# Kernel optimization log

Hardware: AMD Instinct MI355X
Metric: run time of the kernel (lower is better)

## Reference

```python
import jax, jax.numpy as jnp
import numpy as np

N_NODES = 100000
N_EDGES = 1200000
DIM = 64


def _gcn_layer(h, src, dst, norm, W, b):
    # GCNConv: linear -> gather -> normalize -> scatter-add -> bias
    n = h.shape[0]
    h = h @ W                              # [N, D]
    msg = h[src] * norm[:, None]           # [E+N, D] gathered edge messages
    out = jax.ops.segment_sum(msg, dst, num_segments=n)
    return out + b


def setup_inputs() -> dict:
    key = jax.random.key(0)
    ks = jax.random.split(key, 8)
    s = 1.0 / np.sqrt(DIM)
    return {
        "x": jax.random.normal(ks[0], (N_NODES, DIM), jnp.float32),
        "edge_index": jax.random.randint(ks[1], (2, N_EDGES), 0, N_NODES, dtype=jnp.int32),
        "W1": jax.random.normal(ks[2], (DIM, DIM), jnp.float32) * s,
        "b1": jnp.zeros((DIM,), jnp.float32),
        "W2": jax.random.normal(ks[3], (DIM, DIM), jnp.float32) * s,
        "b2": jnp.zeros((DIM,), jnp.float32),
        "W3": jax.random.normal(ks[4], (DIM, DIM), jnp.float32) * s,
        "b3": jnp.zeros((DIM,), jnp.float32),
    }


def reference(x, edge_index, W1, b1, W2, b2, W3, b3):
    n = x.shape[0]
    loops = jnp.arange(n, dtype=edge_index.dtype)
    src = jnp.concatenate([edge_index[0], loops])   # add self-loops (PyG GCNConv default)
    dst = jnp.concatenate([edge_index[1], loops])
    # symmetric degree normalization: norm_e = d^-1/2[src] * d^-1/2[dst]
    deg = jax.ops.segment_sum(jnp.ones(src.shape, x.dtype), dst, num_segments=n)
    dinv = jnp.where(deg > 0, jax.lax.rsqrt(deg), 0.0)
    norm = dinv[src] * dinv[dst]
    h = jax.nn.relu(_gcn_layer(x, src, dst, norm, W1, b1))   # dropout inactive at eval
    h = jax.nn.relu(_gcn_layer(h, src, dst, norm, W2, b2))
    return _gcn_layer(h, src, dst, norm, W3, b3)
```

## Files before the change

### kernel.cpp

```cpp
#include <hip/hip_runtime.h>
#include <math.h>

#define N_NODES 100000
#define N_EDGES 1200000
#define DIM 64
#define ELL_STRIDE 48
#define BNODES 128
#define NBUCKET ((N_NODES + BNODES - 1) / BNODES)
#define BIN_SHIFT 10
#define NBIN ((N_NODES + 1023) >> 10)
#define BIN_CAP 16384
#define CAP 40
#define BIN_BLOCKS 512
#define EPB ((N_EDGES + BIN_BLOCKS - 1) / BIN_BLOCKS)
#define GEMM_BLOCKS ((N_NODES + 63) / 64)
#define GW_BLOCKS (N_NODES / 16)

#define PACK(s, dloc) (((unsigned)(dloc) << 17) | (unsigned)(s))
#define UNPACK_S(p)   ((int)((p) & 0x1FFFF))
#define UNPACK_D(p)   ((int)((p) >> 17))

__device__ __forceinline__ unsigned short f2bf(float f) {
    union { float f; unsigned int u; } v; v.f = f;
    unsigned int r = v.u + 0x7FFF + ((v.u >> 16) & 1);
    return (unsigned short)(r >> 16);
}
__device__ __forceinline__ float bf2f(unsigned short us) {
    return __uint_as_float((unsigned int)us << 16);
}


__global__ void k_init(int* __restrict__ tail) {
    if (threadIdx.x < NBIN) tail[threadIdx.x * 16] = 0;
}


__device__ __forceinline__ void gemm_block(int bid, const float* __restrict__ x,
                                           const float* __restrict__ W,
                                           unsigned short* __restrict__ h,
                                           float4* __restrict__ Xlds) {
    const int tid = threadIdx.x;
    const int lane = tid & 63;

    float wreg[64];
#pragma unroll
    for (int k = 0; k < 64; ++k) wreg[k] = W[k * DIM + lane];

    const int base = bid * 64;
#pragma unroll
    for (int it = 0; it < 4; ++it) {
        int f = tid + it * 256;
        int row = base + (f >> 4);
        if (row >= N_NODES) row = N_NODES - 1;
        Xlds[f] = ((const float4*)x)[row * 16 + (f & 15)];
    }
    __syncthreads();

    const int m0 = (tid >> 6) * 16;
    for (int m = 0; m < 16; ++m) {
        const float4* xr = &Xlds[(m0 + m) * 16];
        float a0 = 0.f, a1 = 0.f, a2 = 0.f, a3 = 0.f;
#pragma unroll
        for (int k4 = 0; k4 < 16; ++k4) {
            float4 xv = xr[k4];
            a0 = fmaf(xv.x, wreg[k4 * 4 + 0], a0);
            a1 = fmaf(xv.y, wreg[k4 * 4 + 1], a1);
            a2 = fmaf(xv.z, wreg[k4 * 4 + 2], a2);
            a3 = fmaf(xv.w, wreg[k4 * 4 + 3], a3);
        }
        int row = base + m0 + m;
        if (row < N_NODES)
            h[(size_t)row * DIM + lane] = f2bf((a0 + a1) + (a2 + a3));
    }
}


__global__ void __launch_bounds__(256) k_pre(const int* __restrict__ ei,
                                             const float* __restrict__ x,
                                             const float* __restrict__ W1,
                                             int* __restrict__ tail,
                                             unsigned* __restrict__ part,
                                             unsigned short* __restrict__ h) {
    __shared__ __align__(16) char smraw[16384];
    __shared__ int lcnt[NBIN];
    __shared__ int gbase[NBIN];
    __shared__ int gcnt[NBIN];

    if (blockIdx.x < GEMM_BLOCKS) {
        gemm_block(blockIdx.x, x, W1, h, (float4*)smraw);
        return;
    }
    unsigned* stg = (unsigned*)smraw;
    const int tid = threadIdx.x;
    for (int i = tid; i < NBIN; i += 256) lcnt[i] = 0;
    __syncthreads();

    const int e0 = (blockIdx.x - GEMM_BLOCKS) * EPB;
    const int eend = (e0 + EPB < N_EDGES) ? e0 + EPB : N_EDGES;
    for (int e = e0 + tid; e < eend; e += 256) {
        int s = ei[e], d = ei[N_EDGES + e];
        int bin = d >> BIN_SHIFT;
        unsigned pk = PACK(s, d & 1023);
        int pos = atomicAdd(&lcnt[bin], 1);
        if (pos < CAP) {
            stg[bin * CAP + pos] = pk;
        } else {
            int gp = atomicAdd(&tail[bin * 16], 1);
            part[(size_t)bin * BIN_CAP + gp] = pk;
        }
    }
    __syncthreads();
    if (tid < NBIN) {
        int c = lcnt[tid]; if (c > CAP) c = CAP;
        gcnt[tid] = c;
        gbase[tid] = c ? atomicAdd(&tail[tid * 16], c) : 0;
    }
    __syncthreads();
    const int wv = tid >> 6, ln = tid & 63;
    for (int b = wv; b < NBIN; b += 4) {
        int c = gcnt[b];
        size_t gbb = (size_t)b * BIN_CAP + gbase[b];
        for (int i = ln; i < c; i += 64)
            part[gbb + i] = stg[b * CAP + i];
    }
}


__global__ void __launch_bounds__(256) k_bucket(const unsigned* __restrict__ part,
                                                const int* __restrict__ tail,
                                                int* __restrict__ ell,
                                                int* __restrict__ deg,
                                                unsigned short* __restrict__ hA,
                                                unsigned short* __restrict__ hB) {
    __shared__ int lcur[BNODES];
    __shared__ int lell[BNODES * ELL_STRIDE];
    const int bucket = blockIdx.x;
    const int tid = threadIdx.x;

    for (int i = tid; i < BNODES; i += 256) lcur[i] = 0;
    __syncthreads();

    const int bin = bucket >> 3;
    const int sub = bucket & 7;
    const int n = tail[bin * 16];
    const unsigned* pb = part + (size_t)bin * BIN_CAP;
    const int node0 = bucket * BNODES;
    for (int i = tid; i < n; i += 256) {
        unsigned p = pb[i];
        unsigned ld = (unsigned)(UNPACK_D(p) - (sub << 7));
        if (ld < BNODES) {
            int pos = atomicAdd(&lcur[ld], 1);
            if (pos < ELL_STRIDE) lell[ld * ELL_STRIDE + pos] = UNPACK_S(p);
        }
    }
    __syncthreads();

    for (int idx = tid; idx < BNODES * ELL_STRIDE; idx += 256) {
        int ln = idx / ELL_STRIDE, sl = idx - ln * ELL_STRIDE;
        int dg = lcur[ln];
        int pe = (dg + 7) & ~7;
        if (pe < 16) pe = 16;
        if (sl >= dg && sl < pe) lell[idx] = N_NODES;
    }
    __syncthreads();

    int4* dst4 = (int4*)(ell + (size_t)bucket * BNODES * ELL_STRIDE);
    const int4* src4 = (const int4*)lell;
    for (int i = tid; i < BNODES * ELL_STRIDE / 4; i += 256) dst4[i] = src4[i];
    for (int i = tid; i < BNODES; i += 256) deg[node0 + i] = lcur[i];

    for (int i = tid; i < BNODES * 8; i += 256) {
        int ln = i >> 3;
        int node = node0 + ln;
        if (node < N_NODES) {
            float dd = rsqrtf((float)(lcur[ln] + 1));
            uint4* p = (uint4*)(hA + (size_t)node * DIM) + (i & 7);
            uint4 v = *p;
            float lo, hi;
            lo = __uint_as_float(v.x << 16) * dd; hi = __uint_as_float(v.x & 0xFFFF0000u) * dd;
            v.x = (unsigned)f2bf(lo) | ((unsigned)f2bf(hi) << 16);
            lo = __uint_as_float(v.y << 16) * dd; hi = __uint_as_float(v.y & 0xFFFF0000u) * dd;
            v.y = (unsigned)f2bf(lo) | ((unsigned)f2bf(hi) << 16);
            lo = __uint_as_float(v.z << 16) * dd; hi = __uint_as_float(v.z & 0xFFFF0000u) * dd;
            v.z = (unsigned)f2bf(lo) | ((unsigned)f2bf(hi) << 16);
            lo = __uint_as_float(v.w << 16) * dd; hi = __uint_as_float(v.w & 0xFFFF0000u) * dd;
            v.w = (unsigned)f2bf(lo) | ((unsigned)f2bf(hi) << 16);
            *p = v;
        }
    }
    if (bucket == 0) {
        if (tid < 8)  ((uint4*)(hA + (size_t)N_NODES * DIM))[tid] = make_uint4(0, 0, 0, 0);
        else if (tid < 16) ((uint4*)(hB + (size_t)N_NODES * DIM))[tid - 8] = make_uint4(0, 0, 0, 0);
    }
}


__global__ void __launch_bounds__(256, 4)
k_gatherW(const unsigned short* __restrict__ h,
          const int* __restrict__ deg,
          const int* __restrict__ ell,
          const float* __restrict__ bvec,
          const float* __restrict__ W,
          unsigned short* __restrict__ hout) {
    __shared__ float sh[16 * 64];
    const int tid = threadIdx.x;
    const int lane = tid & 63;
    const int wv = tid >> 6;
    const int base = blockIdx.x * 16;
    const float bl = bvec[lane];

#pragma unroll 2
    for (int m = 0; m < 4; ++m) {
        int node = base + wv * 4 + m;
        int dg = __builtin_amdgcn_readfirstlane(deg[node]);
        const int* row = ell + (size_t)node * ELL_STRIDE;

        int4 e0 = ((const int4*)row)[0];
        int4 e1 = ((const int4*)row)[1];
        int4 e2 = ((const int4*)row)[2];
        int4 e3 = ((const int4*)row)[3];
        float own = bf2f(h[(size_t)node * DIM + lane]);

        float v0  = bf2f(h[(size_t)e0.x * DIM + lane]);
        float v1  = bf2f(h[(size_t)e0.y * DIM + lane]);
        float v2  = bf2f(h[(size_t)e0.z * DIM + lane]);
        float v3  = bf2f(h[(size_t)e0.w * DIM + lane]);
        float v4  = bf2f(h[(size_t)e1.x * DIM + lane]);
        float v5  = bf2f(h[(size_t)e1.y * DIM + lane]);
        float v6  = bf2f(h[(size_t)e1.z * DIM + lane]);
        float v7  = bf2f(h[(size_t)e1.w * DIM + lane]);
        float v8  = bf2f(h[(size_t)e2.x * DIM + lane]);
        float v9  = bf2f(h[(size_t)e2.y * DIM + lane]);
        float v10 = bf2f(h[(size_t)e2.z * DIM + lane]);
        float v11 = bf2f(h[(size_t)e2.w * DIM + lane]);
        float v12 = bf2f(h[(size_t)e3.x * DIM + lane]);
        float v13 = bf2f(h[(size_t)e3.y * DIM + lane]);
        float v14 = bf2f(h[(size_t)e3.z * DIM + lane]);
        float v15 = bf2f(h[(size_t)e3.w * DIM + lane]);

        float acc = ((own + v0) + (v1 + v2)) + ((v3 + v4) + (v5 + v6))
                  + ((v7 + v8) + (v9 + v10)) + ((v11 + v12) + ((v13 + v14) + v15));

        if (dg > 16) {
            int pe = (dg + 7) & ~7;
            for (int k = 16; k < pe; k += 8) {
                int4 a = *(const int4*)(row + k);
                int4 c = *(const int4*)(row + k + 4);
                float w0 = bf2f(h[(size_t)a.x * DIM + lane]);
                float w1 = bf2f(h[(size_t)a.y * DIM + lane]);
                float w2 = bf2f(h[(size_t)a.z * DIM + lane]);
                float w3 = bf2f(h[(size_t)a.w * DIM + lane]);
                float w4 = bf2f(h[(size_t)c.x * DIM + lane]);
                float w5 = bf2f(h[(size_t)c.y * DIM + lane]);
                float w6 = bf2f(h[(size_t)c.z * DIM + lane]);
                float w7 = bf2f(h[(size_t)c.w * DIM + lane]);
                acc += ((w0 + w1) + (w2 + w3)) + ((w4 + w5) + (w6 + w7));
            }
        }

        float dd = rsqrtf((float)(dg + 1));
        float o = fmaxf(fmaf(acc, dd, bl), 0.f);
        sh[(wv * 4 + m) * 64 + lane] = o;
    }

    float wreg[64];
#pragma unroll
    for (int k = 0; k < 64; ++k) wreg[k] = W[k * DIM + lane];

#pragma unroll
    for (int m = 0; m < 4; ++m) {
        const float4* xr = (const float4*)&sh[(wv * 4 + m) * 64];
        float a0 = 0.f, a1 = 0.f, a2 = 0.f, a3 = 0.f;
#pragma unroll
        for (int k4 = 0; k4 < 16; ++k4) {
            float4 xv = xr[k4];
            a0 = fmaf(xv.x, wreg[k4 * 4 + 0], a0);
            a1 = fmaf(xv.y, wreg[k4 * 4 + 1], a1);
            a2 = fmaf(xv.z, wreg[k4 * 4 + 2], a2);
            a3 = fmaf(xv.w, wreg[k4 * 4 + 3], a3);
        }
        int rown = base + wv * 4 + m;
        float res = (a0 + a1) + (a2 + a3);
        res *= rsqrtf((float)(deg[rown] + 1));
        hout[(size_t)rown * DIM + lane] = f2bf(res);
    }
}


__global__ void k_gatherF(const unsigned short* __restrict__ h,
                          const int* __restrict__ deg,
                          const int* __restrict__ ell, const float* __restrict__ b,
                          float* __restrict__ out) {
    int node = blockIdx.x * 4 + (threadIdx.x >> 6);
    const int lane = threadIdx.x & 63;
    int dg = __builtin_amdgcn_readfirstlane(deg[node]);
    const int* row = ell + (size_t)node * ELL_STRIDE;

    int4 e0 = ((const int4*)row)[0];
    int4 e1 = ((const int4*)row)[1];
    int4 e2 = ((const int4*)row)[2];
    int4 e3 = ((const int4*)row)[3];
    float own = bf2f(h[(size_t)node * DIM + lane]);

    float v0  = bf2f(h[(size_t)e0.x * DIM + lane]);
    float v1  = bf2f(h[(size_t)e0.y * DIM + lane]);
    float v2  = bf2f(h[(size_t)e0.z * DIM + lane]);
    float v3  = bf2f(h[(size_t)e0.w * DIM + lane]);
    float v4  = bf2f(h[(size_t)e1.x * DIM + lane]);
    float v5  = bf2f(h[(size_t)e1.y * DIM + lane]);
    float v6  = bf2f(h[(size_t)e1.z * DIM + lane]);
    float v7  = bf2f(h[(size_t)e1.w * DIM + lane]);
    float v8  = bf2f(h[(size_t)e2.x * DIM + lane]);
    float v9  = bf2f(h[(size_t)e2.y * DIM + lane]);
    float v10 = bf2f(h[(size_t)e2.z * DIM + lane]);
    float v11 = bf2f(h[(size_t)e2.w * DIM + lane]);
    float v12 = bf2f(h[(size_t)e3.x * DIM + lane]);
    float v13 = bf2f(h[(size_t)e3.y * DIM + lane]);
    float v14 = bf2f(h[(size_t)e3.z * DIM + lane]);
    float v15 = bf2f(h[(size_t)e3.w * DIM + lane]);

    float acc = ((own + v0) + (v1 + v2)) + ((v3 + v4) + (v5 + v6))
              + ((v7 + v8) + (v9 + v10)) + ((v11 + v12) + ((v13 + v14) + v15));

    if (dg > 16) {
        int pe = (dg + 7) & ~7;
        for (int k = 16; k < pe; k += 8) {
            int4 a = *(const int4*)(row + k);
            int4 c = *(const int4*)(row + k + 4);
            float w0 = bf2f(h[(size_t)a.x * DIM + lane]);
            float w1 = bf2f(h[(size_t)a.y * DIM + lane]);
            float w2 = bf2f(h[(size_t)a.z * DIM + lane]);
            float w3 = bf2f(h[(size_t)a.w * DIM + lane]);
            float w4 = bf2f(h[(size_t)c.x * DIM + lane]);
            float w5 = bf2f(h[(size_t)c.y * DIM + lane]);
            float w6 = bf2f(h[(size_t)c.z * DIM + lane]);
            float w7 = bf2f(h[(size_t)c.w * DIM + lane]);
            acc += ((w0 + w1) + (w2 + w3)) + ((w4 + w5) + (w6 + w7));
        }
    }

    float dd = rsqrtf((float)(dg + 1));
    out[(size_t)node * DIM + lane] = fmaf(acc, dd, b[lane]);
}


extern "C" void kernel_launch(void* const* d_in, const int* in_sizes, int n_in,
                              void* d_out, int out_size, void* d_ws, size_t ws_size,
                              hipStream_t stream) {
    const float* x   = (const float*)d_in[0];
    const int*   ei  = (const int*)d_in[1];
    const float* W1  = (const float*)d_in[2];
    const float* b1  = (const float*)d_in[3];
    const float* W2  = (const float*)d_in[4];
    const float* b2  = (const float*)d_in[5];
    const float* W3  = (const float*)d_in[6];
    const float* b3  = (const float*)d_in[7];
    float* out = (float*)d_out;

    char* ws = (char*)d_ws;
    int*            deg   = (int*)ws;
    int*            tailp = (int*)(ws + 0x70000);
    int*            ell   = (int*)(ws + 0xD00000);
    unsigned short* hbufA = (unsigned short*)(ws + 0x2000000);
    unsigned short* hbufB = (unsigned short*)(ws + 0x2D00000);
    unsigned*       part  = (unsigned*)(ws + 0x2D00000);

    k_init<<<1, 128, 0, stream>>>(tailp);

    k_pre<<<GEMM_BLOCKS + BIN_BLOCKS, 256, 0, stream>>>(ei, x, W1, tailp, part, hbufA);
    k_bucket<<<NBUCKET, 256, 0, stream>>>(part, tailp, ell, deg, hbufA, hbufB);

    k_gatherW<<<GW_BLOCKS, 256, 0, stream>>>(hbufA, deg, ell, b1, W2, hbufB);
    k_gatherW<<<GW_BLOCKS, 256, 0, stream>>>(hbufB, deg, ell, b2, W3, hbufA);
    k_gatherF<<<N_NODES / 4, 256, 0, stream>>>(hbufA, deg, ell, b3, out);
}
```

Before: 267.5 us.

## Use bf16x3 MFMA for fused GEMM and pre-scaled ELL byte offsets

The per-node dense 64x64 transform in the fused gather kernel is replaced by split-bf16 (hi/lo) MFMA 16x16x32 instructions, with the aggregated rows staged in XOR-swizzled LDS. Precision is kept close to fp32 by adding three cross terms. ELL entries now hold pre-shifted byte offsets (index<<7), so the gather loads skip the 64-bit multiply and address arithmetic. This cuts VALU work and register pressure from the 64-element weight register array. The cost is an extra barrier and the bf16 split conversion overhead.

Result: faster. 246.0 us (-8.0%).

```diff
diff --git a/kernel.cpp b/kernel.cpp
--- a/kernel.cpp
+++ b/kernel.cpp
@@ -20,6 +20,9 @@
 #define UNPACK_S(p)   ((int)((p) & 0x1FFFF))
 #define UNPACK_D(p)   ((int)((p) >> 17))
 
+typedef __attribute__((ext_vector_type(8))) short bf16x8;
+typedef __attribute__((ext_vector_type(4))) float f32x4;
+
 __device__ __forceinline__ unsigned short f2bf(float f) {
     union { float f; unsigned int u; } v; v.f = f;
     unsigned int r = v.u + 0x7FFF + ((v.u >> 16) & 1);
@@ -28,6 +31,8 @@
 __device__ __forceinline__ float bf2f(unsigned short us) {
     return __uint_as_float((unsigned int)us << 16);
 }
+
+#define LDH(boff) bf2f(*(const unsigned short*)((const char*)h + ((unsigned)(boff) + bo)))
 
 
 __global__ void k_init(int* __restrict__ tail) {
@@ -150,7 +155,7 @@
         unsigned ld = (unsigned)(UNPACK_D(p) - (sub << 7));
         if (ld < BNODES) {
             int pos = atomicAdd(&lcur[ld], 1);
-            if (pos < ELL_STRIDE) lell[ld * ELL_STRIDE + pos] = UNPACK_S(p);
+            if (pos < ELL_STRIDE) lell[ld * ELL_STRIDE + pos] = UNPACK_S(p) << 7;
         }
     }
     __syncthreads();
@@ -160,7 +165,7 @@
         int dg = lcur[ln];
         int pe = (dg + 7) & ~7;
         if (pe < 16) pe = 16;
-        if (sl >= dg && sl < pe) lell[idx] = N_NODES;
+        if (sl >= dg && sl < pe) lell[idx] = N_NODES << 7;
     }
     __syncthreads();
 
@@ -202,12 +207,13 @@
           const float* __restrict__ bvec,
           const float* __restrict__ W,
           unsigned short* __restrict__ hout) {
-    __shared__ float sh[16 * 64];
+    __shared__ unsigned short shb[2048];
     const int tid = threadIdx.x;
     const int lane = tid & 63;
     const int wv = tid >> 6;
     const int base = blockIdx.x * 16;
     const float bl = bvec[lane];
+    const unsigned bo = 2u * (unsigned)lane;
 
 #pragma unroll 2
     for (int m = 0; m < 4; ++m) {
@@ -219,24 +225,24 @@
         int4 e1 = ((const int4*)row)[1];
         int4 e2 = ((const int4*)row)[2];
         int4 e3 = ((const int4*)row)[3];
-        float own = bf2f(h[(size_t)node * DIM + lane]);
-
-        float v0  = bf2f(h[(size_t)e0.x * DIM + lane]);
-        float v1  = bf2f(h[(size_t)e0.y * DIM + lane]);
-        float v2  = bf2f(h[(size_t)e0.z * DIM + lane]);
-        float v3  = bf2f(h[(size_t)e0.w * DIM + lane]);
-        float v4  = bf2f(h[(size_t)e1.x * DIM + lane]);
-        float v5  = bf2f(h[(size_t)e1.y * DIM + lane]);
-        float v6  = bf2f(h[(size_t)e1.z * DIM + lane]);
-        float v7  = bf2f(h[(size_t)e1.w * DIM + lane]);
-        float v8  = bf2f(h[(size_t)e2.x * DIM + lane]);
-        float v9  = bf2f(h[(size_t)e2.y * DIM + lane]);
-        float v10 = bf2f(h[(size_t)e2.z * DIM + lane]);
-        float v11 = bf2f(h[(size_t)e2.w * DIM + lane]);
-        float v12 = bf2f(h[(size_t)e3.x * DIM + lane]);
-        float v13 = bf2f(h[(size_t)e3.y * DIM + lane]);
-        float v14 = bf2f(h[(size_t)e3.z * DIM + lane]);
-        float v15 = bf2f(h[(size_t)e3.w * DIM + lane]);
+        float own = LDH((unsigned)node * 128u);
+
+        float v0  = LDH(e0.x);
+        float v1  = LDH(e0.y);
+        float v2  = LDH(e0.z);
+        float v3  = LDH(e0.w);
+        float v4  = LDH(e1.x);
+        float v5  = LDH(e1.y);
+        float v6  = LDH(e1.z);
+        float v7  = LDH(e1.w);
+        float v8  = LDH(e2.x);
+        float v9  = LDH(e2.y);
+        float v10 = LDH(e2.z);
+        float v11 = LDH(e2.w);
+        float v12 = LDH(e3.x);
+        float v13 = LDH(e3.y);
+        float v14 = LDH(e3.z);
+        float v15 = LDH(e3.w);
 
         float acc = ((own + v0) + (v1 + v2)) + ((v3 + v4) + (v5 + v6))
                   + ((v7 + v8) + (v9 + v10)) + ((v11 + v12) + ((v13 + v14) + v15));
@@ -246,43 +252,62 @@
             for (int k = 16; k < pe; k += 8) {
                 int4 a = *(const int4*)(row + k);
                 int4 c = *(const int4*)(row + k + 4);
-                float w0 = bf2f(h[(size_t)a.x * DIM + lane]);
-                float w1 = bf2f(h[(size_t)a.y * DIM + lane]);
-                float w2 = bf2f(h[(size_t)a.z * DIM + lane]);
-                float w3 = bf2f(h[(size_t)a.w * DIM + lane]);
-                float w4 = bf2f(h[(size_t)c.x * DIM + lane]);
-                float w5 = bf2f(h[(size_t)c.y * DIM + lane]);
-                float w6 = bf2f(h[(size_t)c.z * DIM + lane]);
-                float w7 = bf2f(h[(size_t)c.w * DIM + lane]);
+                float w0 = LDH(a.x);
+                float w1 = LDH(a.y);
+                float w2 = LDH(a.z);
+                float w3 = LDH(a.w);
+                float w4 = LDH(c.x);
+                float w5 = LDH(c.y);
+                float w6 = LDH(c.z);
+                float w7 = LDH(c.w);
                 acc += ((w0 + w1) + (w2 + w3)) + ((w4 + w5) + (w6 + w7));
             }
         }
 
         float dd = rsqrtf((float)(dg + 1));
         float o = fmaxf(fmaf(acc, dd, bl), 0.f);
-        sh[(wv * 4 + m) * 64 + lane] = o;
-    }
-
-    float wreg[64];
+        unsigned short oh = f2bf(o);
+        unsigned short ol = f2bf(o - bf2f(oh));
+        int r16 = wv * 4 + m;
+        int pc = r16 * 64 + (((lane >> 3) ^ (r16 & 7)) << 3) + (lane & 7);
+        shb[pc] = oh;
+        shb[1024 + pc] = ol;
+    }
+    __syncthreads();
+
+    const int bcol = wv * 16 + (lane & 15);
+    const int g = lane >> 4;
+    bf16x8 bh0, bl0, bh1, bl1;
 #pragma unroll
-    for (int k = 0; k < 64; ++k) wreg[k] = W[k * DIM + lane];
+    for (int j = 0; j < 8; ++j) {
+        float w0 = W[(g * 8 + j) * DIM + bcol];
+        float w1 = W[(g * 8 + j + 32) * DIM + bcol];
+        unsigned short h0 = f2bf(w0);
+        unsigned short h1 = f2bf(w1);
+        bh0[j] = (short)h0; bl0[j] = (short)f2bf(w0 - bf2f(h0));
+        bh1[j] = (short)h1; bl1[j] = (short)f2bf(w1 - bf2f(h1));
+    }
+
+    const int arow = lane & 15;
+    const int cs = arow & 7;
+    bf16x8 ah0 = *(const bf16x8*)&shb[arow * 64 + ((g ^ cs) << 3)];
+    bf16x8 ah1 = *(const bf16x8*)&shb[arow * 64 + (((g + 4) ^ cs) << 3)];
+    bf16x8 al0 = *(const bf16x8*)&shb[1024 + arow * 64 + ((g ^ cs) << 3)];
+    bf16x8 al1 = *(const bf16x8*)&shb[1024 + arow * 64 + (((g + 4) ^ cs) << 3)];
+
+    f32x4 acc = {0.f, 0.f, 0.f, 0.f};
+    acc = __builtin_amdgcn_mfma_f32_16x16x32_bf16(ah0, bh0, acc, 0, 0, 0);
+    acc = __builtin_amdgcn_mfma_f32_16x16x32_bf16(ah1, bh1, acc, 0, 0, 0);
+    acc = __builtin_amdgcn_mfma_f32_16x16x32_bf16(al0, bh0, acc, 0, 0, 0);
+    acc = __builtin_amdgcn_mfma_f32_16x16x32_bf16(al1, bh1, acc, 0, 0, 0);
+    acc = __builtin_amdgcn_mfma_f32_16x16x32_bf16(ah0, bl0, acc, 0, 0, 0);
+    acc = __builtin_amdgcn_mfma_f32_16x16x32_bf16(ah1, bl1, acc, 0, 0, 0);
 
 #pragma unroll
-    for (int m = 0; m < 4; ++m) {
-        const float4* xr = (const float4*)&sh[(wv * 4 + m) * 64];
-        float a0 = 0.f, a1 = 0.f, a2 = 0.f, a3 = 0.f;
-#pragma unroll
-        for (int k4 = 0; k4 < 16; ++k4) {
-            float4 xv = xr[k4];
-            a0 = fmaf(xv.x, wreg[k4 * 4 + 0], a0);
-            a1 = fmaf(xv.y, wreg[k4 * 4 + 1], a1);
-            a2 = fmaf(xv.z, wreg[k4 * 4 + 2], a2);
-            a3 = fmaf(xv.w, wreg[k4 * 4 + 3], a3);
-        }
-        int rown = base + wv * 4 + m;
-        float res = (a0 + a1) + (a2 + a3);
-        res *= rsqrtf((float)(deg[rown] + 1));
-        hout[(size_t)rown * DIM + lane] = f2bf(res);
+    for (int r = 0; r < 4; ++r) {
+        int rr = g * 4 + r;
+        float res = acc[r] * rsqrtf((float)(deg[base + rr] + 1));
+        hout[(size_t)(base + rr) * DIM + wv * 16 + (lane & 15)] = f2bf(res);
     }
 }
 
@@ -293,6 +318,7 @@
                           float* __restrict__ out) {
     int node = blockIdx.x * 4 + (threadIdx.x >> 6);
     const int lane = threadIdx.x & 63;
+    const unsigned bo = 2u * (unsigned)lane;
     int dg = __builtin_amdgcn_readfirstlane(deg[node]);
     const int* row = ell + (size_t)node * ELL_STRIDE;
 
@@ -300,24 +326,24 @@
     int4 e1 = ((const int4*)row)[1];
     int4 e2 = ((const int4*)row)[2];
     int4 e3 = ((const int4*)row)[3];
-    float own = bf2f(h[(size_t)node * DIM + lane]);
-
-    float v0  = bf2f(h[(size_t)e0.x * DIM + lane]);
-    float v1  = bf2f(h[(size_t)e0.y * DIM + lane]);
-    float v2  = bf2f(h[(size_t)e0.z * DIM + lane]);
-    float v3  = bf2f(h[(size_t)e0.w * DIM + lane]);
-    float v4  = bf2f(h[(size_t)e1.x * DIM + lane]);
-    float v5  = bf2f(h[(size_t)e1.y * DIM + lane]);
-    float v6  = bf2f(h[(size_t)e1.z * DIM + lane]);
-    float v7  = bf2f(h[(size_t)e1.w * DIM + lane]);
-    float v8  = bf2f(h[(size_t)e2.x * DIM + lane]);
-    float v9  = bf2f(h[(size_t)e2.y * DIM + lane]);
-    float v10 = bf2f(h[(size_t)e2.z * DIM + lane]);
-    float v11 = bf2f(h[(size_t)e2.w * DIM + lane]);
-    float v12 = bf2f(h[(size_t)e3.x * DIM + lane]);
-    float v13 = bf2f(h[(size_t)e3.y * DIM + lane]);
-    float v14 = bf2f(h[(size_t)e3.z * DIM + lane]);
-    float v15 = bf2f(h[(size_t)e3.w * DIM + lane]);
+    float own = LDH((unsigned)node * 128u);
+
+    float v0  = LDH(e0.x);
+    float v1  = LDH(e0.y);
+    float v2  = LDH(e0.z);
+    float v3  = LDH(e0.w);
+    float v4  = LDH(e1.x);
+    float v5  = LDH(e1.y);
+    float v6  = LDH(e1.z);
+    float v7  = LDH(e1.w);
+    float v8  = LDH(e2.x);
+    float v9  = LDH(e2.y);
+    float v10 = LDH(e2.z);
+    float v11 = LDH(e2.w);
+    float v12 = LDH(e3.x);
+    float v13 = LDH(e3.y);
+    float v14 = LDH(e3.z);
+    float v15 = LDH(e3.w);
 
     float acc = ((own + v0) + (v1 + v2)) + ((v3 + v4) + (v5 + v6))
               + ((v7 + v8) + (v9 + v10)) + ((v11 + v12) + ((v13 + v14) + v15));
@@ -327,14 +353,14 @@
         for (int k = 16; k < pe; k += 8) {
             int4 a = *(const int4*)(row + k);
             int4 c = *(const int4*)(row + k + 4);
-            float w0 = bf2f(h[(size_t)a.x * DIM + lane]);
-            float w1 = bf2f(h[(size_t)a.y * DIM + lane]);
-            float w2 = bf2f(h[(size_t)a.z * DIM + lane]);
-            float w3 = bf2f(h[(size_t)a.w * DIM + lane]);
-            float w4 = bf2f(h[(size_t)c.x * DIM + lane]);
-            float w5 = bf2f(h[(size_t)c.y * DIM + lane]);
-            float w6 = bf2f(h[(size_t)c.z * DIM + lane]);
-            float w7 = bf2f(h[(size_t)c.w * DIM + lane]);
+            float w0 = LDH(a.x);
+            float w1 = LDH(a.y);
+            float w2 = LDH(a.z);
+            float w3 = LDH(a.w);
+            float w4 = LDH(c.x);
+            float w5 = LDH(c.y);
+            float w6 = LDH(c.z);
+            float w7 = LDH(c.w);
             acc += ((w0 + w1) + (w2 + w3)) + ((w4 + w5) + (w6 + w7));
         }
     }
```
